# Optimization experiments

Hardware: AMD Instinct MI355X
Metric: run time of the kernel (lower is better)

## Reference

```python
import jax, jax.numpy as jnp
import numpy as np
import math

B, C, N, M = 4, 512, 4096, 4096
DA = C // 4
BN_EPS = 1e-5

def setup_inputs() -> dict:
    key = jax.random.key(0)
    ks = jax.random.split(key, 10)
    s = 0.02
    return {
        "x": jax.random.normal(ks[0], (B, C, N), jnp.float32),
        "y": jax.random.normal(ks[1], (B, C, M), jnp.float32),
        # q_conv.weight is tied to k_conv.weight -> single shared [da, C] (no bias)
        "w_qk": jax.random.normal(ks[2], (DA, C), jnp.float32) * s,
        "w_v": jax.random.normal(ks[3], (C, C), jnp.float32) * s,
        "b_v": jax.random.normal(ks[4], (C,), jnp.float32) * s,
        "w_t": jax.random.normal(ks[5], (C, C), jnp.float32) * s,
        "b_t": jax.random.normal(ks[6], (C,), jnp.float32) * s,
        # BatchNorm1d (eval mode: use running stats)
        "gamma": jnp.ones((C,), jnp.float32),
        "beta": jnp.zeros((C,), jnp.float32),
        "run_mean": jax.random.normal(ks[7], (C,), jnp.float32) * 0.1,
        "run_var": jax.random.uniform(ks[8], (C,), jnp.float32, 0.5, 1.5),
    }

def reference(x, y, w_qk, w_v, b_v, w_t, b_t, gamma, beta, run_mean, run_var):
    scale = 1.0 / math.sqrt(DA)
    # 1x1 conv projections (shared q/k weight)
    q = jnp.einsum("dc,bcn->bdn", w_qk, x)                      # [B, da, N]
    k = jnp.einsum("dc,bcm->bdm", w_qk, y)                      # [B, da, M]
    v = jnp.einsum("oc,bcm->bom", w_v, y) + b_v[None, :, None]  # [B, C, M]
    energy = jnp.einsum("bdn,bdm->bnm", q, k) * scale           # [B, N, M]
    attn = jax.nn.softmax(energy, axis=-1)                      # softmax over keys M
    x_s = jnp.einsum("bcm,bnm->bcn", v, attn)                   # [B, C, N]
    x_s = jnp.einsum("oc,bcn->bon", w_t, x_s) + b_t[None, :, None]
    # BatchNorm1d (eval) over channel dim + ReLU
    inv = gamma / jnp.sqrt(run_var + BN_EPS)
    x_s = x_s * inv[None, :, None] + (beta - run_mean * inv)[None, :, None]
    x_s = jax.nn.relu(x_s)
    return jnp.transpose(x_s, (0, 2, 1))                        # [B, N, C]
```

## Files before the change

kernel.cpp:

```cpp
#include <hip/hip_runtime.h>
#include <hip/hip_bf16.h>
#include <stdint.h>

typedef __bf16 bf16;
typedef __bf16 bf16x8 __attribute__((ext_vector_type(8)));
typedef __bf16 bf16x4 __attribute__((ext_vector_type(4)));
typedef float  f32x4  __attribute__((ext_vector_type(4)));

__device__ __forceinline__ int detectf(const void* gma) {
    return (((const uint16_t*)gma)[0] == 0x3F80u) ? 0 : 1;
}

template<typename T> __device__ __forceinline__ bf16x8 load8(const T* p);
template<> __device__ __forceinline__ bf16x8 load8<bf16>(const bf16* p) {
    return *(const bf16x8*)p;
}
template<> __device__ __forceinline__ bf16x8 load8<float>(const float* p) {
    f32x4 a = ((const f32x4*)p)[0];
    f32x4 b = ((const f32x4*)p)[1];
    bf16x8 r;
    #pragma unroll
    for (int m = 0; m < 4; m++) { r[m] = (bf16)a[m]; r[m + 4] = (bf16)b[m]; }
    return r;
}


__device__ __forceinline__ void gld16(bf16* lds, const bf16* g) {
    __builtin_amdgcn_global_load_lds(
        (const __attribute__((address_space(1))) void*)g,
        (__attribute__((address_space(3))) void*)lds, 16, 0, 0);
}

template<int ROWS>
__device__ __forceinline__ void stage(bf16* lds, const bf16* g, int64_t ld, int t) {
    constexpr int NI = ROWS / 32;
    const int w = t >> 6, l = t & 63;
    #pragma unroll
    for (int it = 0; it < NI; it++) {
        const int cb  = (it * 4 + w) * 64;
        const int c   = cb + l;
        const int row = c >> 3, col8 = (c & 7) ^ (row & 7);
        gld16(lds + (int64_t)cb * 8, g + (int64_t)row * ld + col8 * 8);
    }
}

template<int ROWS>
__device__ __forceinline__ void stage512(bf16* lds, const bf16* g, int64_t ld, int t) {
    constexpr int NI = ROWS / 64;
    const int w = t >> 6, l = t & 63;
    #pragma unroll
    for (int it = 0; it < NI; it++) {
        const int cb  = (it * 8 + w) * 64;
        const int c   = cb + l;
        const int row = c >> 3, col8 = (c & 7) ^ (row & 7);
        gld16(lds + (int64_t)cb * 8, g + (int64_t)row * ld + col8 * 8);
    }
}

__device__ __forceinline__ bf16x8 frag(const bf16* lds, int row, int g8) {
    return *(const bf16x8*)&lds[(row << 6) + ((g8 ^ (row & 7)) << 3)];
}

template<int BN_>
__device__ __forceinline__ void core_nt(bf16* As, bf16* Bs,
    const bf16* __restrict__ Ab, const bf16* __restrict__ Bb,
    int64_t ldA, int64_t ldB, int kbeg, int kend, f32x4 (*acc)[BN_ / 32])
{
    const int t = threadIdx.x, lane = t & 63, w = t >> 6;
    const int wi = (w >> 1) * 64, wj = (w & 1) * (BN_ / 2);
    const int quad = lane >> 4, l15 = lane & 15;
    for (int k0 = kbeg; k0 < kend; k0 += 64) {
        stage<128>(As, Ab + k0, ldA, t);
        stage<BN_>(Bs, Bb + k0, ldB, t);
        __syncthreads();
        #pragma unroll
        for (int kk = 0; kk < 64; kk += 32) {
            bf16x8 af[4], bfr[BN_ / 32];
            #pragma unroll
            for (int ti = 0; ti < 4; ti++)
                af[ti] = frag(As, wi + ti * 16 + l15, (kk >> 3) + quad);
            #pragma unroll
            for (int tj = 0; tj < BN_ / 32; tj++)
                bfr[tj] = frag(Bs, wj + tj * 16 + l15, (kk >> 3) + quad);
            #pragma unroll
            for (int ti = 0; ti < 4; ti++)
                #pragma unroll
                for (int tj = 0; tj < BN_ / 32; tj++)
                    acc[ti][tj] = __builtin_amdgcn_mfma_f32_16x16x32_bf16(
                        af[ti], bfr[tj], acc[ti][tj], 0, 0, 0);
        }
        __syncthreads();
    }
}

__global__ __launch_bounds__(256) void k_gemm_plain(
    const bf16* __restrict__ A, const bf16* __restrict__ Bm, bf16* __restrict__ Cc,
    int64_t sAz, int64_t sBz, int64_t sCz, int ldA, int ldB, int ldC, int K)
{
    __shared__ bf16 As[128 * 64];
    __shared__ bf16 Bs[128 * 64];
    const int i0 = blockIdx.y * 128, j0 = blockIdx.x * 128;
    const bf16* Ab = A  + blockIdx.z * sAz + (int64_t)i0 * ldA;
    const bf16* Bb = Bm + blockIdx.z * sBz + (int64_t)j0 * ldB;
    f32x4 acc[4][4] = {};
    core_nt<128>(As, Bs, Ab, Bb, ldA, ldB, 0, K, acc);

    bf16* Cb = Cc + blockIdx.z * sCz;
    const int lane = threadIdx.x & 63, w = threadIdx.x >> 6;
    const int wi = (w >> 1) * 64, wj = (w & 1) * 64, quad = lane >> 4, l15 = lane & 15;
    #pragma unroll
    for (int ti = 0; ti < 4; ti++)
        #pragma unroll
        for (int tj = 0; tj < 4; tj++) {
            const int jg = j0 + wj + tj * 16 + l15;
            #pragma unroll
            for (int r = 0; r < 4; r++)
                Cb[(int64_t)(i0 + wi + ti * 16 + quad * 4 + r) * ldC + jg] = (bf16)acc[ti][tj][r];
        }
}

__global__ __launch_bounds__(256) void k_tr2(
    const void* __restrict__ X, const void* __restrict__ Y,
    bf16* __restrict__ xT, bf16* __restrict__ yT, const void* __restrict__ gma)
{
    __shared__ float tile[64][65];
    const int f = detectf(gma);
    const int z = blockIdx.z, bb = z & 3;
    const void* src = (z < 4) ? X : Y;
    bf16* dst = ((z < 4) ? xT : yT) + (int64_t)bb * 4096 * 512;
    const int s0 = blockIdx.x * 64, c0 = blockIdx.y * 64;
    const int t = threadIdx.x, rl = t >> 4, cl = (t & 15) * 4;
    const int64_t ibase = (int64_t)bb * 512 * 4096;
    #pragma unroll
    for (int p = 0; p < 4; p++) {
        const int r = rl + p * 16;
        if (f) {
            f32x4 v = *(const f32x4*)((const float*)src + ibase + (int64_t)(c0 + r) * 4096 + s0 + cl);
            #pragma unroll
            for (int m = 0; m < 4; m++) tile[r][cl + m] = v[m];
        } else {
            bf16x4 v = *(const bf16x4*)((const bf16*)src + ibase + (int64_t)(c0 + r) * 4096 + s0 + cl);
            #pragma unroll
            for (int m = 0; m < 4; m++) tile[r][cl + m] = (float)v[m];
        }
    }
    __syncthreads();
    #pragma unroll
    for (int p = 0; p < 4; p++) {
        const int srow = rl + p * 16;
        bf16x4 o;
        #pragma unroll
        for (int m = 0; m < 4; m++) o[m] = (bf16)tile[cl + m][srow];
        *(bf16x4*)&dst[(int64_t)(s0 + srow) * 512 + c0 + cl] = o;
    }
}

__global__ __launch_bounds__(256) void k_projg(
    const bf16* __restrict__ xT, const bf16* __restrict__ yT,
    const bf16* __restrict__ wqk, bf16* __restrict__ Qo, bf16* __restrict__ Ko,
    float scale)
{
    __shared__ bf16 As[128 * 64];
    __shared__ bf16 Bs[128 * 64];
    const int z = blockIdx.z, bb = z & 3;
    const bf16* src = ((z < 4) ? xT : yT) + (int64_t)bb * 4096 * 512;
    bf16* dst = ((z < 4) ? Qo : Ko) + (int64_t)bb * 4096 * 128;
    const float sc = (z < 4) ? scale : 1.f;
    const int i0 = blockIdx.y * 128;
    f32x4 acc[4][4] = {};
    core_nt<128>(As, Bs, src + (int64_t)i0 * 512, wqk, 512, 512, 0, 512, acc);

    const int lane = threadIdx.x & 63, w = threadIdx.x >> 6;
    const int wi = (w >> 1) * 64, wj = (w & 1) * 64, quad = lane >> 4, l15 = lane & 15;
    #pragma unroll
    for (int ti = 0; ti < 4; ti++)
        #pragma unroll
        for (int tj = 0; tj < 4; tj++) {
            const int jg = wj + tj * 16 + l15;
            #pragma unroll
            for (int r = 0; r < 4; r++) {
                const int ig = i0 + wi + ti * 16 + quad * 4 + r;
                dst[(int64_t)ig * 128 + jg] = (bf16)(acc[ti][tj][r] * sc);
            }
        }
}

__global__ __launch_bounds__(512, 1) void k_fa(
    const bf16* __restrict__ Qg,
    const bf16* __restrict__ Kg,
    const bf16* __restrict__ Vg,
    void* __restrict__ outB,
    const float* __restrict__ bias2,
    const void* gma, const void* bta, const void* mean, const void* var)
{
    constexpr int DA = 128, M = 4096, N = 4096, MT = 128, NT = M / MT;
    __shared__ bf16 Ks[2][2][128 * 64];
    __shared__ bf16 Ps[64][136];
    __shared__ float Lsh[64];

    const int t = threadIdx.x, lane = t & 63, w = t >> 6;
    const int quad = lane >> 4, l15 = lane & 15;
    const int b = blockIdx.y, n0 = blockIdx.x * 64;
    const int wm = w & 3, wn = w >> 2;

    const bf16* Qb = Qg + ((int64_t)b * N + n0) * DA;
    const bf16* Kb = Kg + (int64_t)b * M * DA;
    const bf16* Vb = Vg + (int64_t)b * 512 * M + (int64_t)(w * 64) * M;

    bf16x8 qf[2][4];
    #pragma unroll
    for (int tj = 0; tj < 2; tj++)
        #pragma unroll
        for (int kk = 0; kk < 4; kk++)
            qf[tj][kk] = *(const bf16x8*)(Qb + (int64_t)(wn * 32 + tj * 16 + l15) * DA
                                          + kk * 32 + quad * 8);

    if (t < 64) Lsh[t] = 0.f;

    f32x4 acc[4][4] = {};

    stage512<128>(&Ks[0][0][0], Kb, DA, t);
    stage512<128>(&Ks[0][1][0], Kb + 64, DA, t);
    bf16x8 vfr[4][4];
    #pragma unroll
    for (int ks = 0; ks < 4; ks++)
        #pragma unroll
        for (int tj = 0; tj < 4; tj++)
            vfr[ks][tj] = *(const bf16x8*)(Vb + (int64_t)(tj * 16 + l15) * M
                                           + ks * 32 + quad * 8);
    __syncthreads();

    for (int mt = 0; mt < NT; mt++) {
        const int cur = mt & 1;
        f32x4 sacc[2][2] = {};
        #pragma unroll
        for (int kk = 0; kk < 4; kk++) {
            bf16x8 kf[2];
            #pragma unroll
            for (int ti = 0; ti < 2; ti++)
                kf[ti] = frag(&Ks[cur][kk >> 1][0], wm * 32 + ti * 16 + l15, (kk & 1) * 4 + quad);
            #pragma unroll
            for (int ti = 0; ti < 2; ti++)
                #pragma unroll
                for (int tj = 0; tj < 2; tj++)
                    sacc[ti][tj] = __builtin_amdgcn_mfma_f32_16x16x32_bf16(
                        kf[ti], qf[tj][kk], sacc[ti][tj], 0, 0, 0);
        }
        float rsum[2] = {0.f, 0.f};
        #pragma unroll
        for (int ti = 0; ti < 2; ti++)
            #pragma unroll
            for (int tj = 0; tj < 2; tj++) {
                const float e0 = __expf(sacc[ti][tj][0]);
                const float e1 = __expf(sacc[ti][tj][1]);
                const float e2 = __expf(sacc[ti][tj][2]);
                const float e3 = __expf(sacc[ti][tj][3]);
                rsum[tj] += (e0 + e1) + (e2 + e3);
                const int n  = wn * 32 + tj * 16 + l15;
                const int mb = wm * 32 + ti * 16 + quad * 4;
                bf16x4 pq;
                pq[0] = (bf16)e0; pq[1] = (bf16)e1; pq[2] = (bf16)e2; pq[3] = (bf16)e3;
                *(bf16x4*)&Ps[n][mb] = pq;
            }
        #pragma unroll
        for (int tj = 0; tj < 2; tj++) {
            float s = rsum[tj];
            s += __shfl_xor(s, 16, 64);
            s += __shfl_xor(s, 32, 64);
            if (quad == 0) atomicAdd(&Lsh[wn * 32 + tj * 16 + l15], s);
        }
        asm volatile("s_waitcnt lgkmcnt(0)" ::: "memory");
        __builtin_amdgcn_s_barrier();
        __builtin_amdgcn_sched_barrier(0);

        if (mt + 1 < NT) {
            const bf16* g = Kb + (int64_t)(mt + 1) * MT * DA;
            stage512<128>(&Ks[cur ^ 1][0][0], g, DA, t);
            stage512<128>(&Ks[cur ^ 1][1][0], g + 64, DA, t);
        }
        __builtin_amdgcn_sched_barrier(0);

        #pragma unroll
        for (int ks = 0; ks < 4; ks++) {
            bf16x8 pf[4];
            #pragma unroll
            for (int ti = 0; ti < 4; ti++)
                pf[ti] = *(const bf16x8*)&Ps[ti * 16 + l15][ks * 32 + quad * 8];
            #pragma unroll
            for (int ti = 0; ti < 4; ti++)
                #pragma unroll
                for (int tj = 0; tj < 4; tj++)
                    acc[ti][tj] = __builtin_amdgcn_mfma_f32_16x16x32_bf16(
                        pf[ti], vfr[ks][tj], acc[ti][tj], 0, 0, 0);
        }
        if (mt + 1 < NT) {
            const bf16* vb = Vb + (int64_t)(mt + 1) * MT;
            #pragma unroll
            for (int ks = 0; ks < 4; ks++)
                #pragma unroll
                for (int tj = 0; tj < 4; tj++)
                    vfr[ks][tj] = *(const bf16x8*)(vb + (int64_t)(tj * 16 + l15) * M
                                                   + ks * 32 + quad * 8);
        }
        asm volatile("s_waitcnt vmcnt(16) lgkmcnt(0)" ::: "memory");
        __builtin_amdgcn_s_barrier();
        __builtin_amdgcn_sched_barrier(0);
    }

    const int f = detectf(gma);
    const int64_t rbase = (int64_t)b * N + n0;
    float inv4[4], add4[4], bj4[4];
    int og[4];
    #pragma unroll
    for (int tj = 0; tj < 4; tj++) {
        const int o = w * 64 + tj * 16 + l15;
        og[tj] = o;
        float g, be, mn, vr;
        if (f) { g  = ((const float*)gma)[o];  be = ((const float*)bta)[o];
                 mn = ((const float*)mean)[o]; vr = ((const float*)var)[o]; }
        else   { g  = (float)((const bf16*)gma)[o];  be = (float)((const bf16*)bta)[o];
                 mn = (float)((const bf16*)mean)[o]; vr = (float)((const bf16*)var)[o]; }
        inv4[tj] = g * rsqrtf(vr + 1e-5f);
        add4[tj] = be - mn * inv4[tj];
        bj4[tj]  = bias2[o];
    }
    #pragma unroll
    for (int ti = 0; ti < 4; ti++)
        #pragma unroll
        for (int r = 0; r < 4; r++) {
            const int nl = ti * 16 + quad * 4 + r;
            const float linv = 1.f / Lsh[nl];
            #pragma unroll
            for (int tj = 0; tj < 4; tj++) {
                float val = (acc[ti][tj][r] * linv + bj4[tj]) * inv4[tj] + add4[tj];
                val = fmaxf(val, 0.f);
                if (f) ((float*)outB)[(rbase + nl) * 512 + og[tj]] = val;
                else   ((bf16*)outB)[(rbase + nl) * 512 + og[tj]] = (bf16)val;
            }
        }
}

__global__ __launch_bounds__(256) void k_prep(
    const void* __restrict__ w_qk, const void* __restrict__ w_t, const void* __restrict__ w_v,
    const void* __restrict__ b_v, const void* __restrict__ b_t,
    bf16* __restrict__ wqkb, bf16* __restrict__ wtb, bf16* __restrict__ wvT,
    float* __restrict__ bias2, const void* __restrict__ gma)
{
    const int f = detectf(gma);
    const int bx = blockIdx.x, t = threadIdx.x;
    if (bx < 160) {
        const void* in = (bx < 32) ? w_qk : w_t;
        bf16* outp     = (bx < 32) ? wqkb : wtb;
        const int64_t idx = ((int64_t)(bx < 32 ? bx : bx - 32) * 256 + t) * 8;
        bf16x8 v = f ? load8<float>((const float*)in + idx)
                     : load8<bf16>((const bf16*)in + idx);
        *(bf16x8*)&outp[idx] = v;
    } else if (bx < 224) {
        __shared__ float tile[64][65];
        const int v = bx - 160;
        const int r0 = (v >> 3) * 64, c0 = (v & 7) * 64;
        const int rl = t >> 4, cl = (t & 15) * 4;
        #pragma unroll
        for (int p = 0; p < 4; p++) {
            const int r = rl + p * 16;
            if (f) {
                f32x4 vv = *(const f32x4*)((const float*)w_v + (int64_t)(r0 + r) * 512 + c0 + cl);
                #pragma unroll
                for (int m = 0; m < 4; m++) tile[r][cl + m] = vv[m];
            } else {
                const bf16* q = (const bf16*)w_v + (int64_t)(r0 + r) * 512 + c0 + cl;
                #pragma unroll
                for (int m = 0; m < 4; m++) tile[r][cl + m] = (float)q[m];
            }
        }
        __syncthreads();
        #pragma unroll
        for (int p = 0; p < 4; p++) {
            const int crow = rl + p * 16;
            bf16x4 o;
            #pragma unroll
            for (int m = 0; m < 4; m++) o[m] = (bf16)tile[cl + m][crow];
            *(bf16x4*)(wvT + (int64_t)(c0 + crow) * 512 + r0 + cl) = o;
        }
    } else {
        const int o = (bx - 224) * 4 + (t >> 6);
        const int lane = t & 63;
        float s = 0.f;
        #pragma unroll
        for (int i = 0; i < 8; i++) {
            const int c = lane + i * 64;
            float bvv, wv_;
            if (f) { bvv = ((const float*)b_v)[c]; wv_ = ((const float*)w_t)[(int64_t)o * 512 + c]; }
            else   { bvv = (float)((const bf16*)b_v)[c]; wv_ = (float)((const bf16*)w_t)[(int64_t)o * 512 + c]; }
            s += bvv * wv_;
        }
        #pragma unroll
        for (int off = 1; off < 64; off <<= 1) s += __shfl_xor(s, off, 64);
        if (lane == 0) {
            const float btv = f ? ((const float*)b_t)[o] : (float)((const bf16*)b_t)[o];
            bias2[o] = s + btv;
        }
    }
}

extern "C" void kernel_launch(void* const* d_in, const int* in_sizes, int n_in,
                              void* d_out, int out_size, void* d_ws, size_t ws_size,
                              hipStream_t stream)
{
    constexpr int B = 4, C = 512, N = 4096, M = 4096, DA = 128;
    const float scale = 0.08838834764831845f;

    const void* x    = d_in[0];
    const void* y    = d_in[1];
    const void* w_qk = d_in[2];
    const void* w_v  = d_in[3];
    const void* b_v  = d_in[4];
    const void* w_t  = d_in[5];
    const void* b_t  = d_in[6];
    const void* gma  = d_in[7];
    const void* bta  = d_in[8];
    const void* rmean= d_in[9];
    const void* rvar = d_in[10];

    char* ws = (char*)d_ws;
    size_t off = 0;
    auto take = [&](size_t nbytes) { size_t p = off; off = (off + nbytes + 255) & ~(size_t)255; return p; };
    float* bias2 = (float*)(ws + take(512 * 4));
    bf16*  wqkb  = (bf16*) (ws + take((size_t)DA * C * 2));
    bf16*  wtb   = (bf16*) (ws + take((size_t)C * C * 2));
    bf16*  wvT   = (bf16*) (ws + take((size_t)C * C * 2));
    bf16*  W     = (bf16*) (ws + take((size_t)C * C * 2));
    bf16*  qT    = (bf16*) (ws + take((size_t)B * N * DA * 2));
    bf16*  kT    = (bf16*) (ws + take((size_t)B * M * DA * 2));
    bf16*  yT    = (bf16*) (ws + take((size_t)B * M * C * 2));
    bf16*  xT    = (bf16*) (ws + take((size_t)B * N * C * 2));
    bf16*  vW    = xT;
    if (off > ws_size) return;

    dim3 blk(256);

    k_prep<<<dim3(352), blk, 0, stream>>>(w_qk, w_t, w_v, b_v, b_t,
                                          wqkb, wtb, wvT, bias2, gma);
    k_tr2<<<dim3(M / 64, C / 64, 2 * B), blk, 0, stream>>>(x, y, xT, yT, gma);
    k_gemm_plain<<<dim3(C / 128, C / 128, 1), blk, 0, stream>>>(
        wtb, wvT, W, 0, 0, 0, C, C, C, C);
    k_projg<<<dim3(1, N / 128, 2 * B), blk, 0, stream>>>(
        xT, yT, wqkb, qT, kT, scale);
    k_gemm_plain<<<dim3(M / 128, C / 128, B), blk, 0, stream>>>(
        W, yT, vW, 0, (int64_t)M * C, (int64_t)C * M, C, C, M, C);
    k_fa<<<dim3(N / 64, B), dim3(512), 0, stream>>>(
        qT, kT, vW, d_out, bias2, gma, bta, rmean, rvar);

    (void)in_sizes; (void)n_in; (void)out_size;
}
```

Measured before the change: 333.6 us.

## Halve attention query tile, raise occupancy, swizzle P buffer, merge prep kernels

The attention kernel now processes 32 queries per block instead of 64. That halves accumulator and V-fragment registers, and launch bounds allow 4 blocks per CU. Row sums stay in registers and are reduced once at the end instead of through per-tile shared atomics. The P staging buffer uses an XOR swizzle, and half the V fragments are loaded just in time under raised priority. Separately, the weight prep and the x/y transposes are merged into one launch, and the W product is merged with the Q/K projections, cutting launch count. Each K tile is now reused across fewer queries, so K traffic per query doubles.

```diff
diff --git a/kernel.cpp b/kernel.cpp
--- a/kernel.cpp
+++ b/kernel.cpp
@@ -119,73 +119,148 @@
         }
 }
 
-__global__ __launch_bounds__(256) void k_tr2(
+__global__ __launch_bounds__(256) void k_prep_tr(
+    const void* __restrict__ w_qk, const void* __restrict__ w_t, const void* __restrict__ w_v,
+    const void* __restrict__ b_v, const void* __restrict__ b_t,
     const void* __restrict__ X, const void* __restrict__ Y,
-    bf16* __restrict__ xT, bf16* __restrict__ yT, const void* __restrict__ gma)
+    bf16* __restrict__ wqkb, bf16* __restrict__ wtb, bf16* __restrict__ wvT,
+    float* __restrict__ bias2, bf16* __restrict__ xT, bf16* __restrict__ yT,
+    const void* __restrict__ gma)
 {
     __shared__ float tile[64][65];
     const int f = detectf(gma);
-    const int z = blockIdx.z, bb = z & 3;
-    const void* src = (z < 4) ? X : Y;
-    bf16* dst = ((z < 4) ? xT : yT) + (int64_t)bb * 4096 * 512;
-    const int s0 = blockIdx.x * 64, c0 = blockIdx.y * 64;
-    const int t = threadIdx.x, rl = t >> 4, cl = (t & 15) * 4;
-    const int64_t ibase = (int64_t)bb * 512 * 4096;
-    #pragma unroll
-    for (int p = 0; p < 4; p++) {
-        const int r = rl + p * 16;
-        if (f) {
-            f32x4 v = *(const f32x4*)((const float*)src + ibase + (int64_t)(c0 + r) * 4096 + s0 + cl);
-            #pragma unroll
-            for (int m = 0; m < 4; m++) tile[r][cl + m] = v[m];
-        } else {
-            bf16x4 v = *(const bf16x4*)((const bf16*)src + ibase + (int64_t)(c0 + r) * 4096 + s0 + cl);
-            #pragma unroll
-            for (int m = 0; m < 4; m++) tile[r][cl + m] = (float)v[m];
-        }
-    }
-    __syncthreads();
-    #pragma unroll
-    for (int p = 0; p < 4; p++) {
-        const int srow = rl + p * 16;
-        bf16x4 o;
-        #pragma unroll
-        for (int m = 0; m < 4; m++) o[m] = (bf16)tile[cl + m][srow];
-        *(bf16x4*)&dst[(int64_t)(s0 + srow) * 512 + c0 + cl] = o;
-    }
-}
-
-__global__ __launch_bounds__(256) void k_projg(
+    const int bx = blockIdx.x, t = threadIdx.x;
+    if (bx < 160) {
+        const void* in = (bx < 32) ? w_qk : w_t;
+        bf16* outp     = (bx < 32) ? wqkb : wtb;
+        const int64_t idx = ((int64_t)(bx < 32 ? bx : bx - 32) * 256 + t) * 8;
+        bf16x8 v = f ? load8<float>((const float*)in + idx)
+                     : load8<bf16>((const bf16*)in + idx);
+        *(bf16x8*)&outp[idx] = v;
+    } else if (bx < 224) {
+        const int v = bx - 160;
+        const int r0 = (v >> 3) * 64, c0 = (v & 7) * 64;
+        const int rl = t >> 4, cl = (t & 15) * 4;
+        #pragma unroll
+        for (int p = 0; p < 4; p++) {
+            const int r = rl + p * 16;
+            if (f) {
+                f32x4 vv = *(const f32x4*)((const float*)w_v + (int64_t)(r0 + r) * 512 + c0 + cl);
+                #pragma unroll
+                for (int m = 0; m < 4; m++) tile[r][cl + m] = vv[m];
+            } else {
+                const bf16* q = (const bf16*)w_v + (int64_t)(r0 + r) * 512 + c0 + cl;
+                #pragma unroll
+                for (int m = 0; m < 4; m++) tile[r][cl + m] = (float)q[m];
+            }
+        }
+        __syncthreads();
+        #pragma unroll
+        for (int p = 0; p < 4; p++) {
+            const int crow = rl + p * 16;
+            bf16x4 o;
+            #pragma unroll
+            for (int m = 0; m < 4; m++) o[m] = (bf16)tile[cl + m][crow];
+            *(bf16x4*)(wvT + (int64_t)(c0 + crow) * 512 + r0 + cl) = o;
+        }
+    } else if (bx < 352) {
+        const int o = (bx - 224) * 4 + (t >> 6);
+        const int lane = t & 63;
+        float s = 0.f;
+        #pragma unroll
+        for (int i = 0; i < 8; i++) {
+            const int c = lane + i * 64;
+            float bvv, wv_;
+            if (f) { bvv = ((const float*)b_v)[c]; wv_ = ((const float*)w_t)[(int64_t)o * 512 + c]; }
+            else   { bvv = (float)((const bf16*)b_v)[c]; wv_ = (float)((const bf16*)w_t)[(int64_t)o * 512 + c]; }
+            s += bvv * wv_;
+        }
+        #pragma unroll
+        for (int off = 1; off < 64; off <<= 1) s += __shfl_xor(s, off, 64);
+        if (lane == 0) {
+            const float btv = f ? ((const float*)b_t)[o] : (float)((const bf16*)b_t)[o];
+            bias2[o] = s + btv;
+        }
+    } else {
+        const int v = bx - 352;
+        const int z = v >> 9, rem = v & 511, bb = z & 3;
+        const void* src = (z < 4) ? X : Y;
+        bf16* dst = ((z < 4) ? xT : yT) + (int64_t)bb * 4096 * 512;
+        const int s0 = (rem >> 3) * 64, c0 = (rem & 7) * 64;
+        const int rl = t >> 4, cl = (t & 15) * 4;
+        const int64_t ibase = (int64_t)bb * 512 * 4096;
+        #pragma unroll
+        for (int p = 0; p < 4; p++) {
+            const int r = rl + p * 16;
+            if (f) {
+                f32x4 vv = *(const f32x4*)((const float*)src + ibase + (int64_t)(c0 + r) * 4096 + s0 + cl);
+                #pragma unroll
+                for (int m = 0; m < 4; m++) tile[r][cl + m] = vv[m];
+            } else {
+                bf16x4 vv = *(const bf16x4*)((const bf16*)src + ibase + (int64_t)(c0 + r) * 4096 + s0 + cl);
+                #pragma unroll
+                for (int m = 0; m < 4; m++) tile[r][cl + m] = (float)vv[m];
+            }
+        }
+        __syncthreads();
+        #pragma unroll
+        for (int p = 0; p < 4; p++) {
+            const int srow = rl + p * 16;
+            bf16x4 o;
+            #pragma unroll
+            for (int m = 0; m < 4; m++) o[m] = (bf16)tile[cl + m][srow];
+            *(bf16x4*)&dst[(int64_t)(s0 + srow) * 512 + c0 + cl] = o;
+        }
+    }
+}
+
+__global__ __launch_bounds__(256) void k_wproj(
+    const bf16* __restrict__ wtb, const bf16* __restrict__ wvT, bf16* __restrict__ Wm,
     const bf16* __restrict__ xT, const bf16* __restrict__ yT,
     const bf16* __restrict__ wqk, bf16* __restrict__ Qo, bf16* __restrict__ Ko,
     float scale)
 {
     __shared__ bf16 As[128 * 64];
     __shared__ bf16 Bs[128 * 64];
-    const int z = blockIdx.z, bb = z & 3;
-    const bf16* src = ((z < 4) ? xT : yT) + (int64_t)bb * 4096 * 512;
-    bf16* dst = ((z < 4) ? Qo : Ko) + (int64_t)bb * 4096 * 128;
-    const float sc = (z < 4) ? scale : 1.f;
-    const int i0 = blockIdx.y * 128;
-    f32x4 acc[4][4] = {};
-    core_nt<128>(As, Bs, src + (int64_t)i0 * 512, wqk, 512, 512, 0, 512, acc);
-
+    const int bx = blockIdx.x;
     const int lane = threadIdx.x & 63, w = threadIdx.x >> 6;
     const int wi = (w >> 1) * 64, wj = (w & 1) * 64, quad = lane >> 4, l15 = lane & 15;
-    #pragma unroll
-    for (int ti = 0; ti < 4; ti++)
-        #pragma unroll
-        for (int tj = 0; tj < 4; tj++) {
-            const int jg = wj + tj * 16 + l15;
-            #pragma unroll
-            for (int r = 0; r < 4; r++) {
-                const int ig = i0 + wi + ti * 16 + quad * 4 + r;
-                dst[(int64_t)ig * 128 + jg] = (bf16)(acc[ti][tj][r] * sc);
-            }
-        }
-}
-
-__global__ __launch_bounds__(512, 1) void k_fa(
+    if (bx < 16) {
+        const int i0 = (bx >> 2) * 128, j0 = (bx & 3) * 128;
+        f32x4 acc[4][4] = {};
+        core_nt<128>(As, Bs, wtb + (int64_t)i0 * 512, wvT + (int64_t)j0 * 512, 512, 512, 0, 512, acc);
+        #pragma unroll
+        for (int ti = 0; ti < 4; ti++)
+            #pragma unroll
+            for (int tj = 0; tj < 4; tj++) {
+                const int jg = j0 + wj + tj * 16 + l15;
+                #pragma unroll
+                for (int r = 0; r < 4; r++)
+                    Wm[(int64_t)(i0 + wi + ti * 16 + quad * 4 + r) * 512 + jg] = (bf16)acc[ti][tj][r];
+            }
+    } else {
+        const int v = bx - 16, z = v >> 5, bb = z & 3;
+        const bf16* src = ((z < 4) ? xT : yT) + (int64_t)bb * 4096 * 512;
+        bf16* dst = ((z < 4) ? Qo : Ko) + (int64_t)bb * 4096 * 128;
+        const float sc = (z < 4) ? scale : 1.f;
+        const int i0 = (v & 31) * 128;
+        f32x4 acc[4][4] = {};
+        core_nt<128>(As, Bs, src + (int64_t)i0 * 512, wqk, 512, 512, 0, 512, acc);
+        #pragma unroll
+        for (int ti = 0; ti < 4; ti++)
+            #pragma unroll
+            for (int tj = 0; tj < 4; tj++) {
+                const int jg = wj + tj * 16 + l15;
+                #pragma unroll
+                for (int r = 0; r < 4; r++) {
+                    const int ig = i0 + wi + ti * 16 + quad * 4 + r;
+                    dst[(int64_t)ig * 128 + jg] = (bf16)(acc[ti][tj][r] * sc);
+                }
+            }
+    }
+}
+
+__global__ __launch_bounds__(512, 4) void k_fa(
     const bf16* __restrict__ Qg,
     const bf16* __restrict__ Kg,
     const bf16* __restrict__ Vg,
@@ -195,35 +270,31 @@
 {
     constexpr int DA = 128, M = 4096, N = 4096, MT = 128, NT = M / MT;
     __shared__ bf16 Ks[2][2][128 * 64];
-    __shared__ bf16 Ps[64][136];
-    __shared__ float Lsh[64];
+    __shared__ bf16 Ps[32 * 128];
 
     const int t = threadIdx.x, lane = t & 63, w = t >> 6;
     const int quad = lane >> 4, l15 = lane & 15;
-    const int b = blockIdx.y, n0 = blockIdx.x * 64;
+    const int b = blockIdx.y, n0 = blockIdx.x * 32;
     const int wm = w & 3, wn = w >> 2;
+    const int rsw = (l15 & 7) << 4;
 
     const bf16* Qb = Qg + ((int64_t)b * N + n0) * DA;
     const bf16* Kb = Kg + (int64_t)b * M * DA;
     const bf16* Vb = Vg + (int64_t)b * 512 * M + (int64_t)(w * 64) * M;
 
-    bf16x8 qf[2][4];
-    #pragma unroll
-    for (int tj = 0; tj < 2; tj++)
-        #pragma unroll
-        for (int kk = 0; kk < 4; kk++)
-            qf[tj][kk] = *(const bf16x8*)(Qb + (int64_t)(wn * 32 + tj * 16 + l15) * DA
-                                          + kk * 32 + quad * 8);
-
-    if (t < 64) Lsh[t] = 0.f;
-
-    f32x4 acc[4][4] = {};
+    bf16x8 qf[4];
+    #pragma unroll
+    for (int kk = 0; kk < 4; kk++)
+        qf[kk] = *(const bf16x8*)(Qb + (int64_t)(wn * 16 + l15) * DA + kk * 32 + quad * 8);
+
+    float rsum = 0.f;
+    f32x4 acc[2][4] = {};
 
     stage512<128>(&Ks[0][0][0], Kb, DA, t);
     stage512<128>(&Ks[0][1][0], Kb + 64, DA, t);
-    bf16x8 vfr[4][4];
-    #pragma unroll
-    for (int ks = 0; ks < 4; ks++)
+    bf16x8 vfr[2][4];
+    #pragma unroll
+    for (int ks = 0; ks < 2; ks++)
         #pragma unroll
         for (int tj = 0; tj < 4; tj++)
             vfr[ks][tj] = *(const bf16x8*)(Vb + (int64_t)(tj * 16 + l15) * M
@@ -232,42 +303,26 @@
 
     for (int mt = 0; mt < NT; mt++) {
         const int cur = mt & 1;
-        f32x4 sacc[2][2] = {};
+        f32x4 sacc[2] = {};
         #pragma unroll
         for (int kk = 0; kk < 4; kk++) {
-            bf16x8 kf[2];
-            #pragma unroll
-            for (int ti = 0; ti < 2; ti++)
-                kf[ti] = frag(&Ks[cur][kk >> 1][0], wm * 32 + ti * 16 + l15, (kk & 1) * 4 + quad);
-            #pragma unroll
-            for (int ti = 0; ti < 2; ti++)
-                #pragma unroll
-                for (int tj = 0; tj < 2; tj++)
-                    sacc[ti][tj] = __builtin_amdgcn_mfma_f32_16x16x32_bf16(
-                        kf[ti], qf[tj][kk], sacc[ti][tj], 0, 0, 0);
-        }
-        float rsum[2] = {0.f, 0.f};
-        #pragma unroll
-        for (int ti = 0; ti < 2; ti++)
-            #pragma unroll
-            for (int tj = 0; tj < 2; tj++) {
-                const float e0 = __expf(sacc[ti][tj][0]);
-                const float e1 = __expf(sacc[ti][tj][1]);
-                const float e2 = __expf(sacc[ti][tj][2]);
-                const float e3 = __expf(sacc[ti][tj][3]);
-                rsum[tj] += (e0 + e1) + (e2 + e3);
-                const int n  = wn * 32 + tj * 16 + l15;
-                const int mb = wm * 32 + ti * 16 + quad * 4;
-                bf16x4 pq;
-                pq[0] = (bf16)e0; pq[1] = (bf16)e1; pq[2] = (bf16)e2; pq[3] = (bf16)e3;
-                *(bf16x4*)&Ps[n][mb] = pq;
-            }
-        #pragma unroll
-        for (int tj = 0; tj < 2; tj++) {
-            float s = rsum[tj];
-            s += __shfl_xor(s, 16, 64);
-            s += __shfl_xor(s, 32, 64);
-            if (quad == 0) atomicAdd(&Lsh[wn * 32 + tj * 16 + l15], s);
+            bf16x8 kf0 = frag(&Ks[cur][kk >> 1][0], wm * 32 + l15,      (kk & 1) * 4 + quad);
+            bf16x8 kf1 = frag(&Ks[cur][kk >> 1][0], wm * 32 + 16 + l15, (kk & 1) * 4 + quad);
+            sacc[0] = __builtin_amdgcn_mfma_f32_16x16x32_bf16(kf0, qf[kk], sacc[0], 0, 0, 0);
+            sacc[1] = __builtin_amdgcn_mfma_f32_16x16x32_bf16(kf1, qf[kk], sacc[1], 0, 0, 0);
+        }
+        #pragma unroll
+        for (int ti = 0; ti < 2; ti++) {
+            const float e0 = __expf(sacc[ti][0]);
+            const float e1 = __expf(sacc[ti][1]);
+            const float e2 = __expf(sacc[ti][2]);
+            const float e3 = __expf(sacc[ti][3]);
+            rsum += (e0 + e1) + (e2 + e3);
+            const int n  = wn * 16 + l15;
+            const int mb = wm * 32 + ti * 16 + quad * 4;
+            bf16x4 pq;
+            pq[0] = (bf16)e0; pq[1] = (bf16)e1; pq[2] = (bf16)e2; pq[3] = (bf16)e3;
+            *(bf16x4*)((char*)Ps + (((n << 8) + (mb << 1)) ^ rsw)) = pq;
         }
         asm volatile("s_waitcnt lgkmcnt(0)" ::: "memory");
         __builtin_amdgcn_s_barrier();
@@ -280,32 +335,52 @@
         }
         __builtin_amdgcn_sched_barrier(0);
 
+        const bf16* vb = Vb + (int64_t)mt * MT;
+        __builtin_amdgcn_s_setprio(1);
+        bf16x8 vt2[4], vt3[4];
+        #pragma unroll
+        for (int tj = 0; tj < 4; tj++)
+            vt2[tj] = *(const bf16x8*)(vb + (int64_t)(tj * 16 + l15) * M + 64 + quad * 8);
+        #pragma unroll
+        for (int tj = 0; tj < 4; tj++)
+            vt3[tj] = *(const bf16x8*)(vb + (int64_t)(tj * 16 + l15) * M + 96 + quad * 8);
         #pragma unroll
         for (int ks = 0; ks < 4; ks++) {
-            bf16x8 pf[4];
-            #pragma unroll
-            for (int ti = 0; ti < 4; ti++)
-                pf[ti] = *(const bf16x8*)&Ps[ti * 16 + l15][ks * 32 + quad * 8];
-            #pragma unroll
-            for (int ti = 0; ti < 4; ti++)
+            bf16x8 pf0 = *(const bf16x8*)((const char*)Ps
+                            + (((l15 << 8) + (ks * 64 + quad * 16)) ^ rsw));
+            bf16x8 pf1 = *(const bf16x8*)((const char*)Ps
+                            + ((((16 + l15) << 8) + (ks * 64 + quad * 16)) ^ rsw));
+            #pragma unroll
+            for (int tj = 0; tj < 4; tj++) {
+                const bf16x8 vf = (ks == 0) ? vfr[0][tj] : (ks == 1) ? vfr[1][tj]
+                                : (ks == 2) ? vt2[tj] : vt3[tj];
+                acc[0][tj] = __builtin_amdgcn_mfma_f32_16x16x32_bf16(pf0, vf, acc[0][tj], 0, 0, 0);
+                acc[1][tj] = __builtin_amdgcn_mfma_f32_16x16x32_bf16(pf1, vf, acc[1][tj], 0, 0, 0);
+            }
+        }
+        __builtin_amdgcn_s_setprio(0);
+        if (mt + 1 < NT) {
+            const bf16* vb2 = Vb + (int64_t)(mt + 1) * MT;
+            #pragma unroll
+            for (int ks = 0; ks < 2; ks++)
                 #pragma unroll
                 for (int tj = 0; tj < 4; tj++)
-                    acc[ti][tj] = __builtin_amdgcn_mfma_f32_16x16x32_bf16(
-                        pf[ti], vfr[ks][tj], acc[ti][tj], 0, 0, 0);
-        }
-        if (mt + 1 < NT) {
-            const bf16* vb = Vb + (int64_t)(mt + 1) * MT;
-            #pragma unroll
-            for (int ks = 0; ks < 4; ks++)
-                #pragma unroll
-                for (int tj = 0; tj < 4; tj++)
-                    vfr[ks][tj] = *(const bf16x8*)(vb + (int64_t)(tj * 16 + l15) * M
+                    vfr[ks][tj] = *(const bf16x8*)(vb2 + (int64_t)(tj * 16 + l15) * M
                                                    + ks * 32 + quad * 8);
         }
-        asm volatile("s_waitcnt vmcnt(16) lgkmcnt(0)" ::: "memory");
+        asm volatile("s_waitcnt vmcnt(8) lgkmcnt(0)" ::: "memory");
         __builtin_amdgcn_s_barrier();
         __builtin_amdgcn_sched_barrier(0);
     }
+
+    float* Lred = (float*)&Ks[0][0][0];
+    {
+        float s = rsum;
+        s += __shfl_xor(s, 16, 64);
+        s += __shfl_xor(s, 32, 64);
+        if (quad == 0) Lred[wm * 32 + wn * 16 + l15] = s;
+    }
+    __syncthreads();
 
     const int f = detectf(gma);
     const int64_t rbase = (int64_t)b * N + n0;
@@ -325,11 +400,12 @@
         bj4[tj]  = bias2[o];
     }
     #pragma unroll
-    for (int ti = 0; ti < 4; ti++)
+    for (int ti = 0; ti < 2; ti++)
         #pragma unroll
         for (int r = 0; r < 4; r++) {
             const int nl = ti * 16 + quad * 4 + r;
-            const float linv = 1.f / Lsh[nl];
+            const float L = Lred[nl] + Lred[32 + nl] + Lred[64 + nl] + Lred[96 + nl];
+            const float linv = 1.f / L;
             #pragma unroll
             for (int tj = 0; tj < 4; tj++) {
                 float val = (acc[ti][tj][r] * linv + bj4[tj]) * inv4[tj] + add4[tj];
@@ -338,69 +414,6 @@
                 else   ((bf16*)outB)[(rbase + nl) * 512 + og[tj]] = (bf16)val;
             }
         }
-}
-
-__global__ __launch_bounds__(256) void k_prep(
-    const void* __restrict__ w_qk, const void* __restrict__ w_t, const void* __restrict__ w_v,
-    const void* __restrict__ b_v, const void* __restrict__ b_t,
-    bf16* __restrict__ wqkb, bf16* __restrict__ wtb, bf16* __restrict__ wvT,
-    float* __restrict__ bias2, const void* __restrict__ gma)
-{
-    const int f = detectf(gma);
-    const int bx = blockIdx.x, t = threadIdx.x;
-    if (bx < 160) {
-        const void* in = (bx < 32) ? w_qk : w_t;
-        bf16* outp     = (bx < 32) ? wqkb : wtb;
-        const int64_t idx = ((int64_t)(bx < 32 ? bx : bx - 32) * 256 + t) * 8;
-        bf16x8 v = f ? load8<float>((const float*)in + idx)
-                     : load8<bf16>((const bf16*)in + idx);
-        *(bf16x8*)&outp[idx] = v;
-    } else if (bx < 224) {
-        __shared__ float tile[64][65];
-        const int v = bx - 160;
-        const int r0 = (v >> 3) * 64, c0 = (v & 7) * 64;
-        const int rl = t >> 4, cl = (t & 15) * 4;
-        #pragma unroll
-        for (int p = 0; p < 4; p++) {
-            const int r = rl + p * 16;
-            if (f) {
-                f32x4 vv = *(const f32x4*)((const float*)w_v + (int64_t)(r0 + r) * 512 + c0 + cl);
-                #pragma unroll
-                for (int m = 0; m < 4; m++) tile[r][cl + m] = vv[m];
-            } else {
-                const bf16* q = (const bf16*)w_v + (int64_t)(r0 + r) * 512 + c0 + cl;
-                #pragma unroll
-                for (int m = 0; m < 4; m++) tile[r][cl + m] = (float)q[m];
-            }
-        }
-        __syncthreads();
-        #pragma unroll
-        for (int p = 0; p < 4; p++) {
-            const int crow = rl + p * 16;
-            bf16x4 o;
-            #pragma unroll
-            for (int m = 0; m < 4; m++) o[m] = (bf16)tile[cl + m][crow];
-            *(bf16x4*)(wvT + (int64_t)(c0 + crow) * 512 + r0 + cl) = o;
-        }
-    } else {
-        const int o = (bx - 224) * 4 + (t >> 6);
-        const int lane = t & 63;
-        float s = 0.f;
-        #pragma unroll
-        for (int i = 0; i < 8; i++) {
-            const int c = lane + i * 64;
-            float bvv, wv_;
-            if (f) { bvv = ((const float*)b_v)[c]; wv_ = ((const float*)w_t)[(int64_t)o * 512 + c]; }
-            else   { bvv = (float)((const bf16*)b_v)[c]; wv_ = (float)((const bf16*)w_t)[(int64_t)o * 512 + c]; }
-            s += bvv * wv_;
-        }
-        #pragma unroll
-        for (int off = 1; off < 64; off <<= 1) s += __shfl_xor(s, off, 64);
-        if (lane == 0) {
-            const float btv = f ? ((const float*)b_t)[o] : (float)((const bf16*)b_t)[o];
-            bias2[o] = s + btv;
-        }
-    }
 }
 
 extern "C" void kernel_launch(void* const* d_in, const int* in_sizes, int n_in,
@@ -439,16 +452,12 @@
 
     dim3 blk(256);
 
-    k_prep<<<dim3(352), blk, 0, stream>>>(w_qk, w_t, w_v, b_v, b_t,
-                                          wqkb, wtb, wvT, bias2, gma);
-    k_tr2<<<dim3(M / 64, C / 64, 2 * B), blk, 0, stream>>>(x, y, xT, yT, gma);
-    k_gemm_plain<<<dim3(C / 128, C / 128, 1), blk, 0, stream>>>(
-        wtb, wvT, W, 0, 0, 0, C, C, C, C);
-    k_projg<<<dim3(1, N / 128, 2 * B), blk, 0, stream>>>(
-        xT, yT, wqkb, qT, kT, scale);
+    k_prep_tr<<<dim3(4448), blk, 0, stream>>>(w_qk, w_t, w_v, b_v, b_t, x, y,
+                                              wqkb, wtb, wvT, bias2, xT, yT, gma);
+    k_wproj<<<dim3(272), blk, 0, stream>>>(wtb, wvT, W, xT, yT, wqkb, qT, kT, scale);
     k_gemm_plain<<<dim3(M / 128, C / 128, B), blk, 0, stream>>>(
         W, yT, vW, 0, (int64_t)M * C, (int64_t)C * M, C, C, M, C);
-    k_fa<<<dim3(N / 64, B), dim3(512), 0, stream>>>(
+    k_fa<<<dim3(N / 32, B), dim3(512), 0, stream>>>(
         qT, kT, vW, d_out, bias2, gma, bta, rmean, rvar);
 
     (void)in_sizes; (void)n_in; (void)out_size;
```

After: 401.9 us. +20.5%, slower.

## Software-pipeline attention QK and softmax with PV, merge prep kernels

Applied to the files above, without the earlier changes.

The attention kernel now computes scores and the exponentiation for the next key tile while the current tile's probabilities are multiplied with V. This uses double-buffered P in shared memory and prefetches K two tiles ahead, which should let MFMA work overlap the exp and LDS traffic. Row sums are kept in registers and reduced once at the end, replacing per-tile shared atomics. Separately, the prep, transpose, weight-GEMM and Q/K projection kernels are merged into two launches to cut launch overhead, at the cost of more register pressure and more complex waitcnt logic.

```diff
diff --git a/kernel.cpp b/kernel.cpp
--- a/kernel.cpp
+++ b/kernel.cpp
@@ -119,70 +119,145 @@
         }
 }
 
-__global__ __launch_bounds__(256) void k_tr2(
+__global__ __launch_bounds__(256) void k_prep_tr(
+    const void* __restrict__ w_qk, const void* __restrict__ w_t, const void* __restrict__ w_v,
+    const void* __restrict__ b_v, const void* __restrict__ b_t,
     const void* __restrict__ X, const void* __restrict__ Y,
-    bf16* __restrict__ xT, bf16* __restrict__ yT, const void* __restrict__ gma)
+    bf16* __restrict__ wqkb, bf16* __restrict__ wtb, bf16* __restrict__ wvT,
+    float* __restrict__ bias2, bf16* __restrict__ xT, bf16* __restrict__ yT,
+    const void* __restrict__ gma)
 {
     __shared__ float tile[64][65];
     const int f = detectf(gma);
-    const int z = blockIdx.z, bb = z & 3;
-    const void* src = (z < 4) ? X : Y;
-    bf16* dst = ((z < 4) ? xT : yT) + (int64_t)bb * 4096 * 512;
-    const int s0 = blockIdx.x * 64, c0 = blockIdx.y * 64;
-    const int t = threadIdx.x, rl = t >> 4, cl = (t & 15) * 4;
-    const int64_t ibase = (int64_t)bb * 512 * 4096;
-    #pragma unroll
-    for (int p = 0; p < 4; p++) {
-        const int r = rl + p * 16;
-        if (f) {
-            f32x4 v = *(const f32x4*)((const float*)src + ibase + (int64_t)(c0 + r) * 4096 + s0 + cl);
-            #pragma unroll
-            for (int m = 0; m < 4; m++) tile[r][cl + m] = v[m];
-        } else {
-            bf16x4 v = *(const bf16x4*)((const bf16*)src + ibase + (int64_t)(c0 + r) * 4096 + s0 + cl);
-            #pragma unroll
-            for (int m = 0; m < 4; m++) tile[r][cl + m] = (float)v[m];
-        }
-    }
-    __syncthreads();
-    #pragma unroll
-    for (int p = 0; p < 4; p++) {
-        const int srow = rl + p * 16;
-        bf16x4 o;
-        #pragma unroll
-        for (int m = 0; m < 4; m++) o[m] = (bf16)tile[cl + m][srow];
-        *(bf16x4*)&dst[(int64_t)(s0 + srow) * 512 + c0 + cl] = o;
-    }
-}
-
-__global__ __launch_bounds__(256) void k_projg(
+    const int bx = blockIdx.x, t = threadIdx.x;
+    if (bx < 160) {
+        const void* in = (bx < 32) ? w_qk : w_t;
+        bf16* outp     = (bx < 32) ? wqkb : wtb;
+        const int64_t idx = ((int64_t)(bx < 32 ? bx : bx - 32) * 256 + t) * 8;
+        bf16x8 v = f ? load8<float>((const float*)in + idx)
+                     : load8<bf16>((const bf16*)in + idx);
+        *(bf16x8*)&outp[idx] = v;
+    } else if (bx < 224) {
+        const int v = bx - 160;
+        const int r0 = (v >> 3) * 64, c0 = (v & 7) * 64;
+        const int rl = t >> 4, cl = (t & 15) * 4;
+        #pragma unroll
+        for (int p = 0; p < 4; p++) {
+            const int r = rl + p * 16;
+            if (f) {
+                f32x4 vv = *(const f32x4*)((const float*)w_v + (int64_t)(r0 + r) * 512 + c0 + cl);
+                #pragma unroll
+                for (int m = 0; m < 4; m++) tile[r][cl + m] = vv[m];
+            } else {
+                const bf16* q = (const bf16*)w_v + (int64_t)(r0 + r) * 512 + c0 + cl;
+                #pragma unroll
+                for (int m = 0; m < 4; m++) tile[r][cl + m] = (float)q[m];
+            }
+        }
+        __syncthreads();
+        #pragma unroll
+        for (int p = 0; p < 4; p++) {
+            const int crow = rl + p * 16;
+            bf16x4 o;
+            #pragma unroll
+            for (int m = 0; m < 4; m++) o[m] = (bf16)tile[cl + m][crow];
+            *(bf16x4*)(wvT + (int64_t)(c0 + crow) * 512 + r0 + cl) = o;
+        }
+    } else if (bx < 352) {
+        const int o = (bx - 224) * 4 + (t >> 6);
+        const int lane = t & 63;
+        float s = 0.f;
+        #pragma unroll
+        for (int i = 0; i < 8; i++) {
+            const int c = lane + i * 64;
+            float bvv, wv_;
+            if (f) { bvv = ((const float*)b_v)[c]; wv_ = ((const float*)w_t)[(int64_t)o * 512 + c]; }
+            else   { bvv = (float)((const bf16*)b_v)[c]; wv_ = (float)((const bf16*)w_t)[(int64_t)o * 512 + c]; }
+            s += bvv * wv_;
+        }
+        #pragma unroll
+        for (int off = 1; off < 64; off <<= 1) s += __shfl_xor(s, off, 64);
+        if (lane == 0) {
+            const float btv = f ? ((const float*)b_t)[o] : (float)((const bf16*)b_t)[o];
+            bias2[o] = s + btv;
+        }
+    } else {
+        const int v = bx - 352;
+        const int z = v >> 9, rem = v & 511, bb = z & 3;
+        const void* src = (z < 4) ? X : Y;
+        bf16* dst = ((z < 4) ? xT : yT) + (int64_t)bb * 4096 * 512;
+        const int s0 = (rem >> 3) * 64, c0 = (rem & 7) * 64;
+        const int rl = t >> 4, cl = (t & 15) * 4;
+        const int64_t ibase = (int64_t)bb * 512 * 4096;
+        #pragma unroll
+        for (int p = 0; p < 4; p++) {
+            const int r = rl + p * 16;
+            if (f) {
+                f32x4 vv = *(const f32x4*)((const float*)src + ibase + (int64_t)(c0 + r) * 4096 + s0 + cl);
+                #pragma unroll
+                for (int m = 0; m < 4; m++) tile[r][cl + m] = vv[m];
+            } else {
+                bf16x4 vv = *(const bf16x4*)((const bf16*)src + ibase + (int64_t)(c0 + r) * 4096 + s0 + cl);
+                #pragma unroll
+                for (int m = 0; m < 4; m++) tile[r][cl + m] = (float)vv[m];
+            }
+        }
+        __syncthreads();
+        #pragma unroll
+        for (int p = 0; p < 4; p++) {
+            const int srow = rl + p * 16;
+            bf16x4 o;
+            #pragma unroll
+            for (int m = 0; m < 4; m++) o[m] = (bf16)tile[cl + m][srow];
+            *(bf16x4*)&dst[(int64_t)(s0 + srow) * 512 + c0 + cl] = o;
+        }
+    }
+}
+
+__global__ __launch_bounds__(256) void k_wproj(
+    const bf16* __restrict__ wtb, const bf16* __restrict__ wvT, bf16* __restrict__ Wm,
     const bf16* __restrict__ xT, const bf16* __restrict__ yT,
     const bf16* __restrict__ wqk, bf16* __restrict__ Qo, bf16* __restrict__ Ko,
     float scale)
 {
     __shared__ bf16 As[128 * 64];
     __shared__ bf16 Bs[128 * 64];
-    const int z = blockIdx.z, bb = z & 3;
-    const bf16* src = ((z < 4) ? xT : yT) + (int64_t)bb * 4096 * 512;
-    bf16* dst = ((z < 4) ? Qo : Ko) + (int64_t)bb * 4096 * 128;
-    const float sc = (z < 4) ? scale : 1.f;
-    const int i0 = blockIdx.y * 128;
-    f32x4 acc[4][4] = {};
-    core_nt<128>(As, Bs, src + (int64_t)i0 * 512, wqk, 512, 512, 0, 512, acc);
-
+    const int bx = blockIdx.x;
     const int lane = threadIdx.x & 63, w = threadIdx.x >> 6;
     const int wi = (w >> 1) * 64, wj = (w & 1) * 64, quad = lane >> 4, l15 = lane & 15;
-    #pragma unroll
-    for (int ti = 0; ti < 4; ti++)
-        #pragma unroll
-        for (int tj = 0; tj < 4; tj++) {
-            const int jg = wj + tj * 16 + l15;
-            #pragma unroll
-            for (int r = 0; r < 4; r++) {
-                const int ig = i0 + wi + ti * 16 + quad * 4 + r;
-                dst[(int64_t)ig * 128 + jg] = (bf16)(acc[ti][tj][r] * sc);
-            }
-        }
+    if (bx < 16) {
+        const int i0 = (bx >> 2) * 128, j0 = (bx & 3) * 128;
+        f32x4 acc[4][4] = {};
+        core_nt<128>(As, Bs, wtb + (int64_t)i0 * 512, wvT + (int64_t)j0 * 512, 512, 512, 0, 512, acc);
+        #pragma unroll
+        for (int ti = 0; ti < 4; ti++)
+            #pragma unroll
+            for (int tj = 0; tj < 4; tj++) {
+                const int jg = j0 + wj + tj * 16 + l15;
+                #pragma unroll
+                for (int r = 0; r < 4; r++)
+                    Wm[(int64_t)(i0 + wi + ti * 16 + quad * 4 + r) * 512 + jg] = (bf16)acc[ti][tj][r];
+            }
+    } else {
+        const int v = bx - 16, z = v >> 5, bb = z & 3;
+        const bf16* src = ((z < 4) ? xT : yT) + (int64_t)bb * 4096 * 512;
+        bf16* dst = ((z < 4) ? Qo : Ko) + (int64_t)bb * 4096 * 128;
+        const float sc = (z < 4) ? scale : 1.f;
+        const int i0 = (v & 31) * 128;
+        f32x4 acc[4][4] = {};
+        core_nt<128>(As, Bs, src + (int64_t)i0 * 512, wqk, 512, 512, 0, 512, acc);
+        #pragma unroll
+        for (int ti = 0; ti < 4; ti++)
+            #pragma unroll
+            for (int tj = 0; tj < 4; tj++) {
+                const int jg = wj + tj * 16 + l15;
+                #pragma unroll
+                for (int r = 0; r < 4; r++) {
+                    const int ig = i0 + wi + ti * 16 + quad * 4 + r;
+                    dst[(int64_t)ig * 128 + jg] = (bf16)(acc[ti][tj][r] * sc);
+                }
+            }
+    }
 }
 
 __global__ __launch_bounds__(512, 1) void k_fa(
@@ -195,8 +270,7 @@
 {
     constexpr int DA = 128, M = 4096, N = 4096, MT = 128, NT = M / MT;
     __shared__ bf16 Ks[2][2][128 * 64];
-    __shared__ bf16 Ps[64][136];
-    __shared__ float Lsh[64];
+    __shared__ bf16 Ps[2][64][136];
 
     const int t = threadIdx.x, lane = t & 63, w = t >> 6;
     const int quad = lane >> 4, l15 = lane & 15;
@@ -215,12 +289,13 @@
             qf[tj][kk] = *(const bf16x8*)(Qb + (int64_t)(wn * 32 + tj * 16 + l15) * DA
                                           + kk * 32 + quad * 8);
 
-    if (t < 64) Lsh[t] = 0.f;
-
+    float rsum[2] = {0.f, 0.f};
     f32x4 acc[4][4] = {};
 
     stage512<128>(&Ks[0][0][0], Kb, DA, t);
     stage512<128>(&Ks[0][1][0], Kb + 64, DA, t);
+    stage512<128>(&Ks[1][0][0], Kb + (int64_t)MT * DA, DA, t);
+    stage512<128>(&Ks[1][1][0], Kb + (int64_t)MT * DA + 64, DA, t);
     bf16x8 vfr[4][4];
     #pragma unroll
     for (int ks = 0; ks < 4; ks++)
@@ -228,17 +303,18 @@
         for (int tj = 0; tj < 4; tj++)
             vfr[ks][tj] = *(const bf16x8*)(Vb + (int64_t)(tj * 16 + l15) * M
                                            + ks * 32 + quad * 8);
-    __syncthreads();
-
-    for (int mt = 0; mt < NT; mt++) {
-        const int cur = mt & 1;
+    asm volatile("s_waitcnt vmcnt(16)" ::: "memory");
+    __builtin_amdgcn_s_barrier();
+    __builtin_amdgcn_sched_barrier(0);
+
+    {
         f32x4 sacc[2][2] = {};
         #pragma unroll
         for (int kk = 0; kk < 4; kk++) {
             bf16x8 kf[2];
             #pragma unroll
             for (int ti = 0; ti < 2; ti++)
-                kf[ti] = frag(&Ks[cur][kk >> 1][0], wm * 32 + ti * 16 + l15, (kk & 1) * 4 + quad);
+                kf[ti] = frag(&Ks[0][kk >> 1][0], wm * 32 + ti * 16 + l15, (kk & 1) * 4 + quad);
             #pragma unroll
             for (int ti = 0; ti < 2; ti++)
                 #pragma unroll
@@ -246,7 +322,6 @@
                     sacc[ti][tj] = __builtin_amdgcn_mfma_f32_16x16x32_bf16(
                         kf[ti], qf[tj][kk], sacc[ti][tj], 0, 0, 0);
         }
-        float rsum[2] = {0.f, 0.f};
         #pragma unroll
         for (int ti = 0; ti < 2; ti++)
             #pragma unroll
@@ -260,32 +335,46 @@
                 const int mb = wm * 32 + ti * 16 + quad * 4;
                 bf16x4 pq;
                 pq[0] = (bf16)e0; pq[1] = (bf16)e1; pq[2] = (bf16)e2; pq[3] = (bf16)e3;
-                *(bf16x4*)&Ps[n][mb] = pq;
-            }
-        #pragma unroll
-        for (int tj = 0; tj < 2; tj++) {
-            float s = rsum[tj];
-            s += __shfl_xor(s, 16, 64);
-            s += __shfl_xor(s, 32, 64);
-            if (quad == 0) atomicAdd(&Lsh[wn * 32 + tj * 16 + l15], s);
-        }
-        asm volatile("s_waitcnt lgkmcnt(0)" ::: "memory");
-        __builtin_amdgcn_s_barrier();
-        __builtin_amdgcn_sched_barrier(0);
-
+                *(bf16x4*)&Ps[0][n][mb] = pq;
+            }
+    }
+    asm volatile("s_waitcnt lgkmcnt(0)" ::: "memory");
+    __builtin_amdgcn_s_barrier();
+    __builtin_amdgcn_sched_barrier(0);
+
+    for (int mt = 0; mt < NT; mt++) {
+        const int cur = mt & 1, nxt = cur ^ 1;
+
+        if (mt + 2 < NT) {
+            const bf16* g = Kb + (int64_t)(mt + 2) * MT * DA;
+            stage512<128>(&Ks[cur][0][0], g, DA, t);
+            stage512<128>(&Ks[cur][1][0], g + 64, DA, t);
+        }
+        __builtin_amdgcn_sched_barrier(0x38F);
+
+        f32x4 sacc[2][2] = {};
         if (mt + 1 < NT) {
-            const bf16* g = Kb + (int64_t)(mt + 1) * MT * DA;
-            stage512<128>(&Ks[cur ^ 1][0][0], g, DA, t);
-            stage512<128>(&Ks[cur ^ 1][1][0], g + 64, DA, t);
-        }
-        __builtin_amdgcn_sched_barrier(0);
+            #pragma unroll
+            for (int kk = 0; kk < 4; kk++) {
+                bf16x8 kf[2];
+                #pragma unroll
+                for (int ti = 0; ti < 2; ti++)
+                    kf[ti] = frag(&Ks[nxt][kk >> 1][0], wm * 32 + ti * 16 + l15, (kk & 1) * 4 + quad);
+                #pragma unroll
+                for (int ti = 0; ti < 2; ti++)
+                    #pragma unroll
+                    for (int tj = 0; tj < 2; tj++)
+                        sacc[ti][tj] = __builtin_amdgcn_mfma_f32_16x16x32_bf16(
+                            kf[ti], qf[tj][kk], sacc[ti][tj], 0, 0, 0);
+            }
+        }
 
         #pragma unroll
         for (int ks = 0; ks < 4; ks++) {
             bf16x8 pf[4];
             #pragma unroll
             for (int ti = 0; ti < 4; ti++)
-                pf[ti] = *(const bf16x8*)&Ps[ti * 16 + l15][ks * 32 + quad * 8];
+                pf[ti] = *(const bf16x8*)&Ps[cur][ti * 16 + l15][ks * 32 + quad * 8];
             #pragma unroll
             for (int ti = 0; ti < 4; ti++)
                 #pragma unroll
@@ -293,19 +382,49 @@
                     acc[ti][tj] = __builtin_amdgcn_mfma_f32_16x16x32_bf16(
                         pf[ti], vfr[ks][tj], acc[ti][tj], 0, 0, 0);
         }
+
         if (mt + 1 < NT) {
-            const bf16* vb = Vb + (int64_t)(mt + 1) * MT;
+            #pragma unroll
+            for (int ti = 0; ti < 2; ti++)
+                #pragma unroll
+                for (int tj = 0; tj < 2; tj++) {
+                    const float e0 = __expf(sacc[ti][tj][0]);
+                    const float e1 = __expf(sacc[ti][tj][1]);
+                    const float e2 = __expf(sacc[ti][tj][2]);
+                    const float e3 = __expf(sacc[ti][tj][3]);
+                    rsum[tj] += (e0 + e1) + (e2 + e3);
+                    const int n  = wn * 32 + tj * 16 + l15;
+                    const int mb = wm * 32 + ti * 16 + quad * 4;
+                    bf16x4 pq;
+                    pq[0] = (bf16)e0; pq[1] = (bf16)e1; pq[2] = (bf16)e2; pq[3] = (bf16)e3;
+                    *(bf16x4*)&Ps[nxt][n][mb] = pq;
+                }
+        }
+
+        if (mt + 1 < NT) {
+            const bf16* vb2 = Vb + (int64_t)(mt + 1) * MT;
             #pragma unroll
             for (int ks = 0; ks < 4; ks++)
                 #pragma unroll
                 for (int tj = 0; tj < 4; tj++)
-                    vfr[ks][tj] = *(const bf16x8*)(vb + (int64_t)(tj * 16 + l15) * M
+                    vfr[ks][tj] = *(const bf16x8*)(vb2 + (int64_t)(tj * 16 + l15) * M
                                                    + ks * 32 + quad * 8);
         }
+
         asm volatile("s_waitcnt vmcnt(16) lgkmcnt(0)" ::: "memory");
         __builtin_amdgcn_s_barrier();
         __builtin_amdgcn_sched_barrier(0);
     }
+
+    float* Lred = (float*)&Ks[0][0][0];
+    #pragma unroll
+    for (int tj = 0; tj < 2; tj++) {
+        float s = rsum[tj];
+        s += __shfl_xor(s, 16, 64);
+        s += __shfl_xor(s, 32, 64);
+        if (quad == 0) Lred[wm * 64 + wn * 32 + tj * 16 + l15] = s;
+    }
+    __syncthreads();
 
     const int f = detectf(gma);
     const int64_t rbase = (int64_t)b * N + n0;
@@ -329,7 +448,8 @@
         #pragma unroll
         for (int r = 0; r < 4; r++) {
             const int nl = ti * 16 + quad * 4 + r;
-            const float linv = 1.f / Lsh[nl];
+            const float L = Lred[nl] + Lred[64 + nl] + Lred[128 + nl] + Lred[192 + nl];
+            const float linv = 1.f / L;
             #pragma unroll
             for (int tj = 0; tj < 4; tj++) {
                 float val = (acc[ti][tj][r] * linv + bj4[tj]) * inv4[tj] + add4[tj];
@@ -338,69 +458,6 @@
                 else   ((bf16*)outB)[(rbase + nl) * 512 + og[tj]] = (bf16)val;
             }
         }
-}
-
-__global__ __launch_bounds__(256) void k_prep(
-    const void* __restrict__ w_qk, const void* __restrict__ w_t, const void* __restrict__ w_v,
-    const void* __restrict__ b_v, const void* __restrict__ b_t,
-    bf16* __restrict__ wqkb, bf16* __restrict__ wtb, bf16* __restrict__ wvT,
-    float* __restrict__ bias2, const void* __restrict__ gma)
-{
-    const int f = detectf(gma);
-    const int bx = blockIdx.x, t = threadIdx.x;
-    if (bx < 160) {
-        const void* in = (bx < 32) ? w_qk : w_t;
-        bf16* outp     = (bx < 32) ? wqkb : wtb;
-        const int64_t idx = ((int64_t)(bx < 32 ? bx : bx - 32) * 256 + t) * 8;
-        bf16x8 v = f ? load8<float>((const float*)in + idx)
-                     : load8<bf16>((const bf16*)in + idx);
-        *(bf16x8*)&outp[idx] = v;
-    } else if (bx < 224) {
-        __shared__ float tile[64][65];
-        const int v = bx - 160;
-        const int r0 = (v >> 3) * 64, c0 = (v & 7) * 64;
-        const int rl = t >> 4, cl = (t & 15) * 4;
-        #pragma unroll
-        for (int p = 0; p < 4; p++) {
-            const int r = rl + p * 16;
-            if (f) {
-                f32x4 vv = *(const f32x4*)((const float*)w_v + (int64_t)(r0 + r) * 512 + c0 + cl);
-                #pragma unroll
-                for (int m = 0; m < 4; m++) tile[r][cl + m] = vv[m];
-            } else {
-                const bf16* q = (const bf16*)w_v + (int64_t)(r0 + r) * 512 + c0 + cl;
-                #pragma unroll
-                for (int m = 0; m < 4; m++) tile[r][cl + m] = (float)q[m];
-            }
-        }
-        __syncthreads();
-        #pragma unroll
-        for (int p = 0; p < 4; p++) {
-            const int crow = rl + p * 16;
-            bf16x4 o;
-            #pragma unroll
-            for (int m = 0; m < 4; m++) o[m] = (bf16)tile[cl + m][crow];
-            *(bf16x4*)(wvT + (int64_t)(c0 + crow) * 512 + r0 + cl) = o;
-        }
-    } else {
-        const int o = (bx - 224) * 4 + (t >> 6);
-        const int lane = t & 63;
-        float s = 0.f;
-        #pragma unroll
-        for (int i = 0; i < 8; i++) {
-            const int c = lane + i * 64;
-            float bvv, wv_;
-            if (f) { bvv = ((const float*)b_v)[c]; wv_ = ((const float*)w_t)[(int64_t)o * 512 + c]; }
-            else   { bvv = (float)((const bf16*)b_v)[c]; wv_ = (float)((const bf16*)w_t)[(int64_t)o * 512 + c]; }
-            s += bvv * wv_;
-        }
-        #pragma unroll
-        for (int off = 1; off < 64; off <<= 1) s += __shfl_xor(s, off, 64);
-        if (lane == 0) {
-            const float btv = f ? ((const float*)b_t)[o] : (float)((const bf16*)b_t)[o];
-            bias2[o] = s + btv;
-        }
-    }
 }
 
 extern "C" void kernel_launch(void* const* d_in, const int* in_sizes, int n_in,
@@ -439,13 +496,9 @@
 
     dim3 blk(256);
 
-    k_prep<<<dim3(352), blk, 0, stream>>>(w_qk, w_t, w_v, b_v, b_t,
-                                          wqkb, wtb, wvT, bias2, gma);
-    k_tr2<<<dim3(M / 64, C / 64, 2 * B), blk, 0, stream>>>(x, y, xT, yT, gma);
-    k_gemm_plain<<<dim3(C / 128, C / 128, 1), blk, 0, stream>>>(
-        wtb, wvT, W, 0, 0, 0, C, C, C, C);
-    k_projg<<<dim3(1, N / 128, 2 * B), blk, 0, stream>>>(
-        xT, yT, wqkb, qT, kT, scale);
+    k_prep_tr<<<dim3(4448), blk, 0, stream>>>(w_qk, w_t, w_v, b_v, b_t, x, y,
+                                              wqkb, wtb, wvT, bias2, xT, yT, gma);
+    k_wproj<<<dim3(272), blk, 0, stream>>>(wtb, wvT, W, xT, yT, wqkb, qT, kT, scale);
     k_gemm_plain<<<dim3(M / 128, C / 128, B), blk, 0, stream>>>(
         W, yT, vW, 0, (int64_t)M * C, (int64_t)C * M, C, C, M, C);
     k_fa<<<dim3(N / 64, B), dim3(512), 0, stream>>>(
```

Result: faster. 304.8 us (-8.6%).
